# Optimization experiments

Measured on AMD Instinct MI355X. Metric: run time of the kernel, lower is better.

Reference implementation:

```python
import jax, jax.numpy as jnp
import numpy as np

N_QUBITS = 8
N_PAIRS = 4
PAIRS = [(2 * p, 2 * p + 1) for p in range(N_PAIRS)]
STRENGTH = 0.8
DIM = 2 ** N_QUBITS


def _apply_1q_full(st, G, q):
    # st: (2,)*n complex64 state, G: [2,2] gate on qubit q (qubit 0 = most significant)
    out = jnp.tensordot(G, st, axes=([1], [q]))
    return jnp.moveaxis(out, 0, q)


def _apply_ctrl_full(st, G, c, t):
    # controlled-G: apply G on target axis t only where control axis c == 1
    s0 = jnp.take(st, 0, axis=c)
    s1 = jnp.take(st, 1, axis=c)
    t2 = t if t < c else t - 1
    s1 = jnp.moveaxis(jnp.tensordot(G, s1, axes=([1], [t2])), 0, t2)
    return jnp.stack([s0, s1], axis=c)


def _entangled_base():
    # |0...0> -> H on q1, partial CNOT (controlled-RX(pi*strength)) on (q1,q2) per pair
    st = jnp.zeros((2,) * N_QUBITS, jnp.complex64).at[(0,) * N_QUBITS].set(1.0)
    H = jnp.array([[1.0, 1.0], [1.0, -1.0]], jnp.complex64) / np.float32(np.sqrt(2.0))
    th = np.float32(np.pi * STRENGTH)
    c, s = np.float32(np.cos(th / 2)), np.float32(np.sin(th / 2))
    RX = jnp.array([[c, -1j * s], [-1j * s, c]], jnp.complex64)
    for q1, q2 in PAIRS:
        st = _apply_1q_full(st, H, q1)
        st = _apply_ctrl_full(st, RX, q1, q2)
    return st.reshape(-1)


def _rx(theta):
    # RX(theta) = [[cos t/2, -i sin t/2], [-i sin t/2, cos t/2]], batched over theta shape
    cz = jnp.cos(0.5 * theta).astype(jnp.complex64)
    sz = (-1j) * jnp.sin(0.5 * theta).astype(jnp.complex64)
    return jnp.stack([jnp.stack([cz, sz], -1), jnpp_stack_fix(sz, cz)], -2) if False else jnp.stack([jnp.stack([cz, sz], -1), jnp.stack([sz, cz], -1)], -2)


def _rz(theta):
    ph = (0.5j) * theta.astype(jnp.complex64)
    e0, e1 = jnp.exp(-ph), jnp.exp(ph)
    z = jnp.zeros_like(e0)
    return jnp.stack([jnp.stack([e0, z], -1), jnp.stack([z, e1], -1)], -2)


def _quantum_scores(k_states):
    # k_states: [B,S,2*n_qubits] -> expected pair-agreement score [B,S]
    B, S, _ = k_states.shape
    k = k_states.reshape(B, S, N_QUBITS, 2)
    eye = jnp.eye(2, dtype=jnp.complex64)
    st = jnp.broadcast_to(_entangled_base(), (B, S, DIM))  # fresh entangled register per (b,j)
    for q in range(N_QUBITS):
        th_x, th_z = k[:, :, q, 0], k[:, :, q, 1]
        Gx = jnp.where((th_x > 0)[..., None, None], _rx(th_x), eye)
        Gz = jnp.where((th_z > 0)[..., None, None], _rz(th_z), eye)
        G = jnp.einsum('bsij,bsjk->bsik', Gz, Gx)  # RX applied first, then RZ
        L = 2 ** q
        R = DIM // (2 * L)
        stv = st.reshape(B, S, L, 2, R)
        st = jnp.einsum('bsij,bsljr->bslir', G, stv).reshape(B, S, DIM)
    probs = (st.real ** 2 + st.imag ** 2).reshape((B, S) + (2,) * N_QUBITS)
    score = jnp.zeros((B, S), probs.dtype)
    for q1, q2 in PAIRS:
        axes = tuple(2 + a for a in range(N_QUBITS) if a not in (q1, q2))
        marg = probs.sum(axis=axes)  # [B,S,2,2] joint marginal of the pair
        score = score + marg[..., 0, 0] + marg[..., 1, 1]  # P(measure equal)
    return score / N_PAIRS


def reference(query, key, value, Wq, bq, Wk, bk, Wv, bv, Wo, bo):
    q_states = query @ Wq + bq  # computed as in original forward (unused by scores)
    k_states = key @ Wk + bk    # [B,S,2*n_qubits]
    v_states = value @ Wv + bv  # [B,S,d_model]
    B, S, _ = k_states.shape
    score = _quantum_scores(k_states)  # [B,S]; deterministic expected agreement
    # original loop makes score[b,i,j] independent of i under independent per-(b,i,j) sims
    attn = jnp.broadcast_to(score[:, None, :], (B, S, S))
    w = jax.nn.softmax(attn, axis=-1)
    out = jnp.einsum('bij,bjd->bid', w, v_states)
    return out @ Wo + bo


def setup_inputs() -> dict:
    rng = jax.random.key(0)
    ks = jax.random.split(rng, 8)
    B, S, D = 8, 2048, 512
    nq2 = 2 * N_QUBITS
    f = jax.random.normal
    return {
        'query': f(ks[0], (B, S, D), jnp.float32),
        'key': f(ks[1], (B, S, D), jnp.float32),
        'value': f(ks[2], (B, S, D), jnp.float32),
        'Wq': f(ks[3], (D, nq2), jnp.float32) * 0.05,
        'bq': jnp.zeros((nq2,), jnp.float32),
        'Wk': f(ks[4], (D, nq2), jnp.float32) * 0.05,
        'bk': jnp.zeros((nq2,), jnp.float32),
        'Wv': f(ks[5], (D, D), jnp.float32) * 0.05,
        'bv': jnp.zeros((D,), jnp.float32),
        'Wo': f(ks[6], (D, D), jnp.float32) * 0.05,
        'bo': jnp.zeros((D,), jnp.float32),
    }
```

## Files before the change

kernel.cpp:

```cpp
#include <hip/hip_runtime.h>
#include <math.h>

#define DEV __device__ __forceinline__

struct C2 { float x, y; };
DEV C2 cmul(C2 a, C2 b){ return {a.x*b.x - a.y*b.y, a.x*b.y + a.y*b.x}; }
DEV C2 cadd(C2 a, C2 b){ return {a.x+b.x, a.y+b.y}; }
DEV C2 cscale(C2 a, float s){ return {a.x*s, a.y*s}; }
DEV C2 cnegi(C2 a){ return {a.y, -a.x}; }

__global__ __launch_bounds__(256) void k_score_wsum(const float* __restrict__ key,
                                                    const float* __restrict__ Wk,
                                                    const float* __restrict__ bk,
                                                    const float* __restrict__ value,
                                                    float* __restrict__ partial,
                                                    float* __restrict__ partialw)
{
    const int c = blockIdx.x;
    const int b = blockIdx.y;
    const int t = threadIdx.x;
    const int lane = t & 63;
    const int wv   = t >> 6;
    const int base = b * 2048 + c * 32;

    __shared__ float wlds[32];
    __shared__ float4 tmp[128];

    float4 wk[8][4];
    #pragma unroll
    for (int jj = 0; jj < 4; ++jj) {
        const float4* w0 = (const float4*)(Wk + (4 * lane + jj) * 16);
        const float4* w1 = (const float4*)(Wk + (256 + 4 * lane + jj) * 16);
        #pragma unroll
        for (int q = 0; q < 4; ++q) { wk[jj][q] = w0[q]; wk[4 + jj][q] = w1[q]; }
    }
    const float bkr = bk[lane & 15];
    const float c0 = 0.30901699437494745f;
    const float s0 = 0.9510565162951535f;

    #pragma unroll 2
    for (int i = 0; i < 8; ++i) {
        const int j = wv * 8 + i;
        const float4* kp = (const float4*)(key + (size_t)(base + j) * 512);
        float4 k0 = kp[lane];
        float4 k1 = kp[64 + lane];
        float el[8] = {k0.x, k0.y, k0.z, k0.w, k1.x, k1.y, k1.z, k1.w};
        float acc[16];
        #pragma unroll
        for (int k = 0; k < 16; ++k) acc[k] = 0.f;
        #pragma unroll
        for (int jr = 0; jr < 8; ++jr) {
            #pragma unroll
            for (int q = 0; q < 4; ++q) {
                acc[4*q+0] = fmaf(el[jr], wk[jr][q].x, acc[4*q+0]);
                acc[4*q+1] = fmaf(el[jr], wk[jr][q].y, acc[4*q+1]);
                acc[4*q+2] = fmaf(el[jr], wk[jr][q].z, acc[4*q+2]);
                acc[4*q+3] = fmaf(el[jr], wk[jr][q].w, acc[4*q+3]);
            }
        }
        #pragma unroll
        for (int s = 0; s < 4; ++s) {
            const int m = 1 << s;
            const int bbit = (lane >> s) & 1;
            #pragma unroll
            for (int jj = 0; jj < (16 >> (s + 1)); ++jj) {
                float send = bbit ? acc[2*jj] : acc[2*jj+1];
                float keep = bbit ? acc[2*jj+1] : acc[2*jj];
                float got  = __shfl_xor(send, m);
                acc[jj] = keep + got;
            }
        }
        float ks = acc[0];
        ks += __shfl_xor(ks, 16);
        ks += __shfl_xor(ks, 32);
        ks += bkr;

        int pp = lane & 3;
        float ax = __shfl(ks, 4*pp+0);
        float az = __shfl(ks, 4*pp+1);
        float bx = __shfl(ks, 4*pp+2);
        float bz = __shfl(ks, 4*pp+3);
        float cxa = 1.f, sxa = 0.f; if (ax > 0.f){ sxa = __sinf(0.5f*ax); cxa = __cosf(0.5f*ax); }
        float cpa = 1.f, spa = 0.f; if (az > 0.f){ spa = __sinf(0.5f*az); cpa = __cosf(0.5f*az); }
        float cxb = 1.f, sxb = 0.f; if (bx > 0.f){ sxb = __sinf(0.5f*bx); cxb = __cosf(0.5f*bx); }
        float cpb = 1.f, spb = 0.f; if (bz > 0.f){ spb = __sinf(0.5f*bz); cpb = __cosf(0.5f*bz); }
        C2 A00{cpa*cxa, -spa*cxa}, A01{-spa*sxa, -cpa*sxa};
        C2 A10{spa*sxa, -cpa*sxa}, A11{ cpa*cxa,  spa*cxa};
        C2 B00{cpb*cxb, -spb*cxb}, B01{-spb*sxb, -cpb*sxb};
        C2 B10{spb*sxb, -cpb*sxb}, B11{ cpb*cxb,  spb*cxb};
        C2 u = cadd(cmul(B00, cadd(A00, cscale(A01, c0))),
                    cscale(cnegi(cmul(A01, B01)), s0));
        C2 v = cadd(cmul(B10, cadd(A10, cscale(A11, c0))),
                    cscale(cnegi(cmul(A11, B11)), s0));
        float ps = u.x*u.x + u.y*u.y + v.x*v.x + v.y*v.y;
        ps += __shfl_xor(ps, 1);
        ps += __shfl_xor(ps, 2);
        if (lane == 0) wlds[j] = __expf(ps * 0.125f);
    }
    __syncthreads();

    const int col4 = t & 127, rg = t >> 7;
    const float4* vbase = (const float4*)value
        + ((size_t)base + rg * 16) * 128 + col4;
    float4 acc = {0.f, 0.f, 0.f, 0.f};
    #pragma unroll 4
    for (int j = 0; j < 16; ++j) {
        float wj = wlds[rg * 16 + j];
        float4 v = vbase[(size_t)j * 128];
        acc.x = fmaf(wj, v.x, acc.x); acc.y = fmaf(wj, v.y, acc.y);
        acc.z = fmaf(wj, v.z, acc.z); acc.w = fmaf(wj, v.w, acc.w);
    }
    if (rg) tmp[col4] = acc;
    __syncthreads();
    if (!rg) {
        float4 o = tmp[col4];
        acc.x += o.x; acc.y += o.y; acc.z += o.z; acc.w += o.w;
        ((float4*)partial)[((size_t)b*64 + c) * 128 + col4] = acc;
    }
    if (t < 32) {
        float s = wlds[t];
        s += __shfl_xor(s, 1);  s += __shfl_xor(s, 2);
        s += __shfl_xor(s, 4);  s += __shfl_xor(s, 8);
        s += __shfl_xor(s, 16);
        if (t == 0) partialw[b * 64 + c] = s;
    }
}

__global__ __launch_bounds__(256) void k_ctx(const float* __restrict__ partial,
                                             const float* __restrict__ partialw,
                                             const float* __restrict__ Wv,
                                             const float* __restrict__ bv,
                                             float* __restrict__ ctx)
{
    int dt = blockIdx.x, b = blockIdx.y, t = threadIdx.x;
    __shared__ float vb[512];
    __shared__ float invS;
    __shared__ float red[256];

    if (t < 64) {
        float s = partialw[b * 64 + t];
        s += __shfl_xor(s, 1);  s += __shfl_xor(s, 2);
        s += __shfl_xor(s, 4);  s += __shfl_xor(s, 8);
        s += __shfl_xor(s, 16); s += __shfl_xor(s, 32);
        if (t == 0) invS = 1.f / s;
    }
    float a0 = 0.f, a1 = 0.f;
    const float* pp = partial + (size_t)b * 64 * 512;
    #pragma unroll 4
    for (int c = 0; c < 64; ++c) {
        a0 += pp[c * 512 + t];
        a1 += pp[c * 512 + 256 + t];
    }
    __syncthreads();
    vb[t] = a0 * invS; vb[t + 256] = a1 * invS;
    __syncthreads();

    int dl = t & 63, q = t >> 6;
    int d = dt * 64 + dl;
    const float* x  = vb + q * 128;
    const float* Wc = Wv + (size_t)(q * 128) * 512 + d;
    float acc = 0.f;
    #pragma unroll 4
    for (int e = 0; e < 128; ++e) acc = fmaf(x[e], Wc[(size_t)e * 512], acc);
    red[t] = acc; __syncthreads();
    if (t < 64)
        ctx[b * 512 + dt * 64 + t] = red[t] + red[t+64] + red[t+128] + red[t+192]
                                   + bv[dt * 64 + t];
}

__global__ __launch_bounds__(256) void k_out(const float* __restrict__ ctx,
                                             const float* __restrict__ Wo,
                                             const float* __restrict__ bo,
                                             float* __restrict__ out)
{
    int dt = blockIdx.x, b = blockIdx.y, is = blockIdx.z, t = threadIdx.x;
    __shared__ float xs[512];
    __shared__ float red[256];
    __shared__ float4 frow4[16];

    xs[t]       = ctx[b * 512 + t];
    xs[t + 256] = ctx[b * 512 + 256 + t];
    __syncthreads();

    int dl = t & 63, q = t >> 6;
    int d = dt * 64 + dl;
    const float* x  = xs + q * 128;
    const float* Wc = Wo + (size_t)(q * 128) * 512 + d;
    float acc = 0.f;
    #pragma unroll 4
    for (int e = 0; e < 128; ++e) acc = fmaf(x[e], Wc[(size_t)e * 512], acc);
    red[t] = acc; __syncthreads();
    if (t < 64)
        ((float*)frow4)[t] = red[t] + red[t+64] + red[t+128] + red[t+192]
                           + bo[dt * 64 + t];
    __syncthreads();

    int col4 = t & 15, r0 = t >> 4;
    float4 val = frow4[col4];
    float4* o4 = (float4*)out + ((size_t)b * 2048 + is * 128) * 128 + dt * 16;
    #pragma unroll
    for (int rr = r0; rr < 128; rr += 16)
        o4[(size_t)rr * 128 + col4] = val;
}

extern "C" void kernel_launch(void* const* d_in, const int* in_sizes, int n_in,
                              void* d_out, int out_size, void* d_ws, size_t ws_size,
                              hipStream_t stream) {
    const float* key   = (const float*)d_in[1];
    const float* value = (const float*)d_in[2];
    const float* Wk    = (const float*)d_in[5];
    const float* bk    = (const float*)d_in[6];
    const float* Wv    = (const float*)d_in[7];
    const float* bv    = (const float*)d_in[8];
    const float* Wo    = (const float*)d_in[9];
    const float* bo    = (const float*)d_in[10];
    float* out = (float*)d_out;
    float* ws  = (float*)d_ws;

    float* partial  = ws;
    float* partialw = ws + 262144;
    float* ctx      = ws + 262656;

    k_score_wsum<<<dim3(64, 8), 256, 0, stream>>>(key, Wk, bk, value,
                                                  partial, partialw);
    k_ctx       <<<dim3(8, 8), 256, 0, stream>>>(partial, partialw, Wv, bv, ctx);
    k_out       <<<dim3(8, 8, 16), 256, 0, stream>>>(ctx, Wo, bo, out);
}
```

Before: 187.9 us.

## Restructure score kernel with prefetch, per-wave value accumulation, and split output broadcast

The score kernel now computes two key rows per iteration with software prefetch of the next rows. Per-row projections go to LDS, and the gate math runs once across the wave (8 rows times 4 pairs per lane) instead of once per row. Value rows are loaded into registers early and accumulated per wave, then reduced across waves in LDS. The ctx reduction uses float4 loads, and the output projection is split from a separate wide broadcast kernel so Wo is no longer recomputed 16 times. The cost is one extra launch and higher register pressure from holding the value rows in registers.

```diff
diff --git a/kernel.cpp b/kernel.cpp
--- a/kernel.cpp
+++ b/kernel.cpp
@@ -22,9 +22,11 @@
     const int lane = t & 63;
     const int wv   = t >> 6;
     const int base = b * 2048 + c * 32;
-
-    __shared__ float wlds[32];
-    __shared__ float4 tmp[128];
+    const int r0   = base + wv * 8;
+
+    __shared__ float  kslds[32][16];
+    __shared__ float4 red[4][128];
+    __shared__ float  wsums[4];
 
     float4 wk[8][4];
     #pragma unroll
@@ -38,24 +40,33 @@
     const float c0 = 0.30901699437494745f;
     const float s0 = 0.9510565162951535f;
 
-    #pragma unroll 2
-    for (int i = 0; i < 8; ++i) {
-        const int j = wv * 8 + i;
-        const float4* kp = (const float4*)(key + (size_t)(base + j) * 512);
-        float4 k0 = kp[lane];
-        float4 k1 = kp[64 + lane];
-        float el[8] = {k0.x, k0.y, k0.z, k0.w, k1.x, k1.y, k1.z, k1.w};
-        float acc[16];
-        #pragma unroll
-        for (int k = 0; k < 16; ++k) acc[k] = 0.f;
+    const float4* kp = (const float4*)(key + (size_t)r0 * 512);
+    float4 a0 = kp[lane],       a1 = kp[64 + lane];
+    float4 b0 = kp[128 + lane], b1 = kp[192 + lane];
+    #pragma unroll
+    for (int i = 0; i < 8; i += 2) {
+        float4 na0, na1, nb0, nb1;
+        if (i < 6) {
+            na0 = kp[(i + 2) * 128 + lane]; na1 = kp[(i + 2) * 128 + 64 + lane];
+            nb0 = kp[(i + 3) * 128 + lane]; nb1 = kp[(i + 3) * 128 + 64 + lane];
+        }
+        float eA[8] = {a0.x, a0.y, a0.z, a0.w, a1.x, a1.y, a1.z, a1.w};
+        float eB[8] = {b0.x, b0.y, b0.z, b0.w, b1.x, b1.y, b1.z, b1.w};
+        float accA[16], accB[16];
+        #pragma unroll
+        for (int k = 0; k < 16; ++k) { accA[k] = 0.f; accB[k] = 0.f; }
         #pragma unroll
         for (int jr = 0; jr < 8; ++jr) {
             #pragma unroll
             for (int q = 0; q < 4; ++q) {
-                acc[4*q+0] = fmaf(el[jr], wk[jr][q].x, acc[4*q+0]);
-                acc[4*q+1] = fmaf(el[jr], wk[jr][q].y, acc[4*q+1]);
-                acc[4*q+2] = fmaf(el[jr], wk[jr][q].z, acc[4*q+2]);
-                acc[4*q+3] = fmaf(el[jr], wk[jr][q].w, acc[4*q+3]);
+                accA[4*q+0] = fmaf(eA[jr], wk[jr][q].x, accA[4*q+0]);
+                accA[4*q+1] = fmaf(eA[jr], wk[jr][q].y, accA[4*q+1]);
+                accA[4*q+2] = fmaf(eA[jr], wk[jr][q].z, accA[4*q+2]);
+                accA[4*q+3] = fmaf(eA[jr], wk[jr][q].w, accA[4*q+3]);
+                accB[4*q+0] = fmaf(eB[jr], wk[jr][q].x, accB[4*q+0]);
+                accB[4*q+1] = fmaf(eB[jr], wk[jr][q].y, accB[4*q+1]);
+                accB[4*q+2] = fmaf(eB[jr], wk[jr][q].z, accB[4*q+2]);
+                accB[4*q+3] = fmaf(eB[jr], wk[jr][q].w, accB[4*q+3]);
             }
         }
         #pragma unroll
@@ -64,66 +75,78 @@
             const int bbit = (lane >> s) & 1;
             #pragma unroll
             for (int jj = 0; jj < (16 >> (s + 1)); ++jj) {
-                float send = bbit ? acc[2*jj] : acc[2*jj+1];
-                float keep = bbit ? acc[2*jj+1] : acc[2*jj];
-                float got  = __shfl_xor(send, m);
-                acc[jj] = keep + got;
+                float sA = bbit ? accA[2*jj] : accA[2*jj+1];
+                float kA = bbit ? accA[2*jj+1] : accA[2*jj];
+                accA[jj] = kA + __shfl_xor(sA, m);
+                float sB = bbit ? accB[2*jj] : accB[2*jj+1];
+                float kB = bbit ? accB[2*jj+1] : accB[2*jj];
+                accB[jj] = kB + __shfl_xor(sB, m);
             }
         }
-        float ks = acc[0];
-        ks += __shfl_xor(ks, 16);
-        ks += __shfl_xor(ks, 32);
-        ks += bkr;
-
-        int pp = lane & 3;
-        float ax = __shfl(ks, 4*pp+0);
-        float az = __shfl(ks, 4*pp+1);
-        float bx = __shfl(ks, 4*pp+2);
-        float bz = __shfl(ks, 4*pp+3);
-        float cxa = 1.f, sxa = 0.f; if (ax > 0.f){ sxa = __sinf(0.5f*ax); cxa = __cosf(0.5f*ax); }
-        float cpa = 1.f, spa = 0.f; if (az > 0.f){ spa = __sinf(0.5f*az); cpa = __cosf(0.5f*az); }
-        float cxb = 1.f, sxb = 0.f; if (bx > 0.f){ sxb = __sinf(0.5f*bx); cxb = __cosf(0.5f*bx); }
-        float cpb = 1.f, spb = 0.f; if (bz > 0.f){ spb = __sinf(0.5f*bz); cpb = __cosf(0.5f*bz); }
-        C2 A00{cpa*cxa, -spa*cxa}, A01{-spa*sxa, -cpa*sxa};
-        C2 A10{spa*sxa, -cpa*sxa}, A11{ cpa*cxa,  spa*cxa};
-        C2 B00{cpb*cxb, -spb*cxb}, B01{-spb*sxb, -cpb*sxb};
-        C2 B10{spb*sxb, -cpb*sxb}, B11{ cpb*cxb,  spb*cxb};
-        C2 u = cadd(cmul(B00, cadd(A00, cscale(A01, c0))),
-                    cscale(cnegi(cmul(A01, B01)), s0));
-        C2 v = cadd(cmul(B10, cadd(A10, cscale(A11, c0))),
-                    cscale(cnegi(cmul(A11, B11)), s0));
-        float ps = u.x*u.x + u.y*u.y + v.x*v.x + v.y*v.y;
-        ps += __shfl_xor(ps, 1);
-        ps += __shfl_xor(ps, 2);
-        if (lane == 0) wlds[j] = __expf(ps * 0.125f);
-    }
-    __syncthreads();
-
-    const int col4 = t & 127, rg = t >> 7;
-    const float4* vbase = (const float4*)value
-        + ((size_t)base + rg * 16) * 128 + col4;
-    float4 acc = {0.f, 0.f, 0.f, 0.f};
-    #pragma unroll 4
-    for (int j = 0; j < 16; ++j) {
-        float wj = wlds[rg * 16 + j];
-        float4 v = vbase[(size_t)j * 128];
-        acc.x = fmaf(wj, v.x, acc.x); acc.y = fmaf(wj, v.y, acc.y);
-        acc.z = fmaf(wj, v.z, acc.z); acc.w = fmaf(wj, v.w, acc.w);
-    }
-    if (rg) tmp[col4] = acc;
-    __syncthreads();
-    if (!rg) {
-        float4 o = tmp[col4];
-        acc.x += o.x; acc.y += o.y; acc.z += o.z; acc.w += o.w;
-        ((float4*)partial)[((size_t)b*64 + c) * 128 + col4] = acc;
-    }
-    if (t < 32) {
-        float s = wlds[t];
-        s += __shfl_xor(s, 1);  s += __shfl_xor(s, 2);
-        s += __shfl_xor(s, 4);  s += __shfl_xor(s, 8);
-        s += __shfl_xor(s, 16);
-        if (t == 0) partialw[b * 64 + c] = s;
-    }
+        float ksA = accA[0];
+        ksA += __shfl_xor(ksA, 16); ksA += __shfl_xor(ksA, 32); ksA += bkr;
+        float ksB = accB[0];
+        ksB += __shfl_xor(ksB, 16); ksB += __shfl_xor(ksB, 32); ksB += bkr;
+        if (lane < 16) {
+            kslds[wv * 8 + i][lane]     = ksA;
+            kslds[wv * 8 + i + 1][lane] = ksB;
+        }
+        if (i < 6) { a0 = na0; a1 = na1; b0 = nb0; b1 = nb1; }
+    }
+
+    const float4* vp = (const float4*)(value + (size_t)r0 * 512);
+    float4 vreg[16];
+    #pragma unroll
+    for (int j = 0; j < 8; ++j) {
+        vreg[2*j]   = vp[j * 128 + lane];
+        vreg[2*j+1] = vp[j * 128 + 64 + lane];
+    }
+
+    const int p  = (lane >> 3) & 3;
+    const int jr = lane & 7;
+    float4 kv = *(const float4*)&kslds[wv * 8 + jr][4 * p];
+    float ax = kv.x, az = kv.y, bx = kv.z, bz = kv.w;
+    float cxa = 1.f, sxa = 0.f; if (ax > 0.f){ sxa = __sinf(0.5f*ax); cxa = __cosf(0.5f*ax); }
+    float cpa = 1.f, spa = 0.f; if (az > 0.f){ spa = __sinf(0.5f*az); cpa = __cosf(0.5f*az); }
+    float cxb = 1.f, sxb = 0.f; if (bx > 0.f){ sxb = __sinf(0.5f*bx); cxb = __cosf(0.5f*bx); }
+    float cpb = 1.f, spb = 0.f; if (bz > 0.f){ spb = __sinf(0.5f*bz); cpb = __cosf(0.5f*bz); }
+    C2 A00{cpa*cxa, -spa*cxa}, A01{-spa*sxa, -cpa*sxa};
+    C2 A10{spa*sxa, -cpa*sxa}, A11{ cpa*cxa,  spa*cxa};
+    C2 B00{cpb*cxb, -spb*cxb}, B01{-spb*sxb, -cpb*sxb};
+    C2 B10{spb*sxb, -cpb*sxb}, B11{ cpb*cxb,  spb*cxb};
+    C2 u = cadd(cmul(B00, cadd(A00, cscale(A01, c0))),
+                cscale(cnegi(cmul(A01, B01)), s0));
+    C2 v = cadd(cmul(B10, cadd(A10, cscale(A11, c0))),
+                cscale(cnegi(cmul(A11, B11)), s0));
+    float ps = u.x*u.x + u.y*u.y + v.x*v.x + v.y*v.y;
+    ps += __shfl_xor(ps, 8);
+    ps += __shfl_xor(ps, 16);
+    float w_all = __expf(ps * 0.125f);
+
+    float sw = w_all;
+    sw += __shfl_xor(sw, 1); sw += __shfl_xor(sw, 2); sw += __shfl_xor(sw, 4);
+    if (lane == 0) wsums[wv] = sw;
+
+    float4 aA = {0.f,0.f,0.f,0.f}, aB = {0.f,0.f,0.f,0.f};
+    #pragma unroll
+    for (int j = 0; j < 8; ++j) {
+        float wj = __shfl(w_all, j);
+        float4 v0 = vreg[2*j], v1 = vreg[2*j+1];
+        aA.x = fmaf(wj, v0.x, aA.x); aA.y = fmaf(wj, v0.y, aA.y);
+        aA.z = fmaf(wj, v0.z, aA.z); aA.w = fmaf(wj, v0.w, aA.w);
+        aB.x = fmaf(wj, v1.x, aB.x); aB.y = fmaf(wj, v1.y, aB.y);
+        aB.z = fmaf(wj, v1.z, aB.z); aB.w = fmaf(wj, v1.w, aB.w);
+    }
+    red[wv][lane] = aA;
+    red[wv][64 + lane] = aB;
+    __syncthreads();
+    if (t < 128) {
+        float4 q0 = red[0][t], q1 = red[1][t], q2 = red[2][t], q3 = red[3][t];
+        float4 o = { q0.x+q1.x+q2.x+q3.x, q0.y+q1.y+q2.y+q3.y,
+                     q0.z+q1.z+q2.z+q3.z, q0.w+q1.w+q2.w+q3.w };
+        ((float4*)partial)[((size_t)b * 64 + c) * 128 + t] = o;
+    }
+    if (t == 0) partialw[b * 64 + c] = wsums[0] + wsums[1] + wsums[2] + wsums[3];
 }
 
 __global__ __launch_bounds__(256) void k_ctx(const float* __restrict__ partial,
@@ -133,9 +156,10 @@
                                              float* __restrict__ ctx)
 {
     int dt = blockIdx.x, b = blockIdx.y, t = threadIdx.x;
-    __shared__ float vb[512];
-    __shared__ float invS;
-    __shared__ float red[256];
+    __shared__ float4 red4[2][128];
+    __shared__ float  vb[512];
+    __shared__ float  red[256];
+    __shared__ float  invS;
 
     if (t < 64) {
         float s = partialw[b * 64 + t];
@@ -144,15 +168,25 @@
         s += __shfl_xor(s, 16); s += __shfl_xor(s, 32);
         if (t == 0) invS = 1.f / s;
     }
-    float a0 = 0.f, a1 = 0.f;
-    const float* pp = partial + (size_t)b * 64 * 512;
-    #pragma unroll 4
-    for (int c = 0; c < 64; ++c) {
-        a0 += pp[c * 512 + t];
-        a1 += pp[c * 512 + 256 + t];
-    }
-    __syncthreads();
-    vb[t] = a0 * invS; vb[t + 256] = a1 * invS;
+    const int col4 = t & 127, cg = t >> 7;
+    const float4* pp4 = (const float4*)partial
+                      + ((size_t)b * 64 + cg * 32) * 128 + col4;
+    float4 a = {0.f, 0.f, 0.f, 0.f};
+    #pragma unroll 8
+    for (int cc = 0; cc < 32; ++cc) {
+        float4 v = pp4[(size_t)cc * 128];
+        a.x += v.x; a.y += v.y; a.z += v.z; a.w += v.w;
+    }
+    red4[cg][col4] = a;
+    __syncthreads();
+    if (t < 128) {
+        float4 q0 = red4[0][t], q1 = red4[1][t];
+        float is = invS;
+        vb[4*t+0] = (q0.x + q1.x) * is;
+        vb[4*t+1] = (q0.y + q1.y) * is;
+        vb[4*t+2] = (q0.z + q1.z) * is;
+        vb[4*t+3] = (q0.w + q1.w) * is;
+    }
     __syncthreads();
 
     int dl = t & 63, q = t >> 6;
@@ -160,7 +194,7 @@
     const float* x  = vb + q * 128;
     const float* Wc = Wv + (size_t)(q * 128) * 512 + d;
     float acc = 0.f;
-    #pragma unroll 4
+    #pragma unroll 8
     for (int e = 0; e < 128; ++e) acc = fmaf(x[e], Wc[(size_t)e * 512], acc);
     red[t] = acc; __syncthreads();
     if (t < 64)
@@ -168,15 +202,14 @@
                                    + bv[dt * 64 + t];
 }
 
-__global__ __launch_bounds__(256) void k_out(const float* __restrict__ ctx,
-                                             const float* __restrict__ Wo,
-                                             const float* __restrict__ bo,
-                                             float* __restrict__ out)
-{
-    int dt = blockIdx.x, b = blockIdx.y, is = blockIdx.z, t = threadIdx.x;
+__global__ __launch_bounds__(256) void k_frow(const float* __restrict__ ctx,
+                                              const float* __restrict__ Wo,
+                                              const float* __restrict__ bo,
+                                              float* __restrict__ frow)
+{
+    int dt = blockIdx.x, b = blockIdx.y, t = threadIdx.x;
     __shared__ float xs[512];
     __shared__ float red[256];
-    __shared__ float4 frow4[16];
 
     xs[t]       = ctx[b * 512 + t];
     xs[t + 256] = ctx[b * 512 + 256 + t];
@@ -187,20 +220,24 @@
     const float* x  = xs + q * 128;
     const float* Wc = Wo + (size_t)(q * 128) * 512 + d;
     float acc = 0.f;
-    #pragma unroll 4
+    #pragma unroll 8
     for (int e = 0; e < 128; ++e) acc = fmaf(x[e], Wc[(size_t)e * 512], acc);
     red[t] = acc; __syncthreads();
     if (t < 64)
-        ((float*)frow4)[t] = red[t] + red[t+64] + red[t+128] + red[t+192]
-                           + bo[dt * 64 + t];
-    __syncthreads();
-
-    int col4 = t & 15, r0 = t >> 4;
-    float4 val = frow4[col4];
-    float4* o4 = (float4*)out + ((size_t)b * 2048 + is * 128) * 128 + dt * 16;
-    #pragma unroll
-    for (int rr = r0; rr < 128; rr += 16)
-        o4[(size_t)rr * 128 + col4] = val;
+        frow[b * 512 + dt * 64 + t] = red[t] + red[t+64] + red[t+128] + red[t+192]
+                                    + bo[dt * 64 + t];
+}
+
+__global__ __launch_bounds__(256) void k_bcast(const float* __restrict__ frow,
+                                               float* __restrict__ out)
+{
+    int s = blockIdx.x, b = blockIdx.y, t = threadIdx.x;
+    const int col4 = t & 127, h = t >> 7;
+    float4 val = ((const float4*)frow)[b * 128 + col4];
+    float4* o4 = (float4*)out
+               + ((size_t)b * 2048 + s * 32 + h * 16) * 128 + col4;
+    #pragma unroll
+    for (int r = 0; r < 16; ++r) o4[(size_t)r * 128] = val;
 }
 
 extern "C" void kernel_launch(void* const* d_in, const int* in_sizes, int n_in,
@@ -220,9 +257,11 @@
     float* partial  = ws;
     float* partialw = ws + 262144;
     float* ctx      = ws + 262656;
+    float* frow     = ws + 266752;
 
     k_score_wsum<<<dim3(64, 8), 256, 0, stream>>>(key, Wk, bk, value,
                                                   partial, partialw);
-    k_ctx       <<<dim3(8, 8), 256, 0, stream>>>(partial, partialw, Wv, bv, ctx);
-    k_out       <<<dim3(8, 8, 16), 256, 0, stream>>>(ctx, Wo, bo, out);
-}
+    k_ctx <<<dim3(8, 8),  256, 0, stream>>>(partial, partialw, Wv, bv, ctx);
+    k_frow<<<dim3(8, 8),  256, 0, stream>>>(ctx, Wo, bo, frow);
+    k_bcast<<<dim3(64, 8), 256, 0, stream>>>(frow, out);
+}
```

Measured after the change: 166.9 us. 1.13x faster.
